# Kernel tuning notes

Hardware: AMD Instinct MI355X
Metric: run time of the kernel (lower is better)

Reference implementation:

```python
import jax, jax.numpy as jnp
import numpy as np
import math

# Module hyperparameters (from init_kwargs)
T_TOTAL = 1.0
NUM_STEPS = 8          # == len(F), number of time-indexed sub-networks (experts)
D = 1024               # feature dim (shape = [D])
DH = 4096              # hidden dim of each expert MLP
B = 4096               # batch size
H_STEP = T_TOTAL / NUM_STEPS
EIGMIN, EIGINIT, EIGMAX = -1.0, 0.0, 1.0   # spectral_limits=None
INV_SIG_099 = math.log(0.99 / (1 - 0.99))  # shifta/shiftb/scales init (learn flags False)


def setup_inputs() -> dict:
    key = jax.random.key(0)
    ks = jax.random.split(key, 8)
    t = jax.random.uniform(ks[0], (B,), dtype=jnp.float32) * T_TOTAL
    y = jax.random.normal(ks[1], (B, D), dtype=jnp.float32)
    # Per-expert 2-layer MLP params, stacked over the expert axis E
    s1 = 1.0 / math.sqrt(D)
    s2 = 1.0 / math.sqrt(DH)
    W1 = jax.random.normal(ks[2], (NUM_STEPS, D, DH), dtype=jnp.float32) * s1
    b1 = jnp.zeros((NUM_STEPS, DH), dtype=jnp.float32)
    W2 = jax.random.normal(ks[3], (NUM_STEPS, DH, D), dtype=jnp.float32) * s2
    b2 = jnp.zeros((NUM_STEPS, D), dtype=jnp.float32)
    scales = jnp.full((1, D), INV_SIG_099, dtype=jnp.float32)
    shifta = jnp.float32(INV_SIG_099)
    shiftb = jnp.float32(INV_SIG_099)
    return {"t": t, "y": y, "W1": W1, "b1": b1, "W2": W2, "b2": b2,
            "scales": scales, "shifta": shifta, "shiftb": shiftb}


def reference(t, y, W1, b1, W2, b2, scales, shifta, shiftb):
    E = W1.shape[0]
    # t2ind: per-sample expert index, clamped to the last expert
    ind = jnp.minimum((t / H_STEP).astype(jnp.int32), E - 1)          # [B]
    # Run every expert on every sample (dense dispatch), then gather per-sample result.
    hid = jnp.tanh(jnp.einsum('bd,edh->ebh', y, W1) + b1[:, None, :])  # [E,B,DH]
    fe = jnp.einsum('ebh,ehd->ebd', hid, W2) + b2[:, None, :]          # [E,B,D]
    f = jnp.take_along_axis(fe, ind[None, :, None].astype(jnp.int32), axis=0)[0]  # [B,D]
    f = jax.nn.sigmoid(scales) * f
    a = EIGINIT + jax.nn.sigmoid(shifta) * (EIGMIN - EIGINIT)
    b = EIGINIT + jax.nn.sigmoid(shiftb) * (EIGMAX - EIGINIT)
    return 0.5 * ((b - a) * f + (a + b) * y)
```

## Files before the change

kernel.cpp:

```cpp
#include <hip/hip_runtime.h>
#include <hip/hip_bf16.h>
#include <math.h>

#define NEXP 8
#define DIM_D 1024
#define DIM_H 4096
#define NB 4096

typedef __attribute__((ext_vector_type(8))) short short8;
typedef __attribute__((ext_vector_type(4))) float floatx4;

__device__ __forceinline__ unsigned short f2bf(float x) {
  __hip_bfloat16 h = __float2bfloat16(x);
  unsigned short u;
  __builtin_memcpy(&u, &h, 2);
  return u;
}
__device__ __forceinline__ unsigned int pack2bf(float a, float b) {
  return (unsigned int)f2bf(a) | ((unsigned int)f2bf(b) << 16);
}

__device__ __forceinline__ void async_copy16(const void* g, void* l) {
  __builtin_amdgcn_global_load_lds(
      (const __attribute__((address_space(1))) unsigned int*)g,
      (__attribute__((address_space(3))) unsigned int*)l, 16, 0, 0);
}

__global__ void setup_kernel(const float* __restrict__ t,
                             int* __restrict__ offs, int* __restrict__ perm) {
  __shared__ int cnt[NEXP];
  __shared__ int cur[NEXP];
  const int tid = threadIdx.x;
  if (tid < NEXP) cnt[tid] = 0;
  __syncthreads();
  for (int i = tid; i < NB; i += 256) {
    int e = (int)(t[i] * 8.0f);
    e = e < 0 ? 0 : (e > NEXP - 1 ? NEXP - 1 : e);
    atomicAdd(&cnt[e], 1);
  }
  __syncthreads();
  if (tid == 0) {
    int s = 0;
    for (int e = 0; e < NEXP; ++e) { offs[e] = s; cur[e] = s; s += cnt[e]; }
    offs[NEXP] = s;
  }
  __syncthreads();
  for (int i = tid; i < NB; i += 256) {
    int e = (int)(t[i] * 8.0f);
    e = e < 0 ? 0 : (e > NEXP - 1 ? NEXP - 1 : e);
    int slot = atomicAdd(&cur[e], 1);
    perm[slot] = i;
  }
}

__global__ __launch_bounds__(256)
void cvt_kernel(const float* __restrict__ in, __hip_bfloat16* __restrict__ out) {
  const long long i = ((long long)blockIdx.x * 256 + threadIdx.x) * 8;
  const float4 a = *(const float4*)(in + i);
  const float4 b = *(const float4*)(in + i + 4);
  unsigned int r[4];
  r[0] = pack2bf(a.x, a.y);
  r[1] = pack2bf(a.z, a.w);
  r[2] = pack2bf(b.x, b.y);
  r[3] = pack2bf(b.z, b.w);
  *(uint4*)(out + i) = *(const uint4*)r;
}

__global__ __launch_bounds__(256)
void transpose_cvt_kernel(const float* __restrict__ in,
                          __hip_bfloat16* __restrict__ out, int R, int C) {
  __shared__ unsigned int wbuf[32 * 69];
  const long long base = (long long)blockIdx.z * R * C;
  const int c0 = blockIdx.x * 64;
  const int r0 = blockIdx.y * 64;
  const int t = threadIdx.x;
  {
    const int p = t >> 3, g = t & 7;
    const float* s0 = in + base + (long long)(r0 + 2 * p) * C + c0 + g * 8;
    const float4 a0 = *(const float4*)(s0);
    const float4 a1 = *(const float4*)(s0 + 4);
    const float4 b0 = *(const float4*)(s0 + C);
    const float4 b1v = *(const float4*)(s0 + C + 4);
    unsigned int* dp = &wbuf[p * 69 + g * 8];
    dp[0] = pack2bf(a0.x, b0.x);
    dp[1] = pack2bf(a0.y, b0.y);
    dp[2] = pack2bf(a0.z, b0.z);
    dp[3] = pack2bf(a0.w, b0.w);
    dp[4] = pack2bf(a1.x, b1v.x);
    dp[5] = pack2bf(a1.y, b1v.y);
    dp[6] = pack2bf(a1.z, b1v.z);
    dp[7] = pack2bf(a1.w, b1v.w);
  }
  __syncthreads();
  {
    const int oc = t >> 2, rq = t & 3;
    __align__(16) unsigned int res[8];
#pragma unroll
    for (int j = 0; j < 8; ++j) res[j] = wbuf[(rq * 8 + j) * 69 + oc];
    __hip_bfloat16* dstp = out + base + (long long)(c0 + oc) * R + r0 + rq * 16;
    *(uint4*)dstp = *(const uint4*)&res[0];
    *(uint4*)(dstp + 8) = *(const uint4*)&res[4];
  }
}

template <int MODE>
__global__ __launch_bounds__(256, 2)
void gemm_kernel(const __hip_bfloat16* __restrict__ A,
                 const __hip_bfloat16* __restrict__ BT,
                 const float* __restrict__ bias,
                 const int* __restrict__ offs, const int* __restrict__ perm,
                 void* __restrict__ dstv,
                 const float* __restrict__ yin,
                 const float* __restrict__ scales,
                 const float* __restrict__ shifta,
                 const float* __restrict__ shiftb,
                 int K, int N) {
  const int e  = blockIdx.y >> 5;
  const int mt = blockIdx.y & 31;
  const int off = offs[e];
  const int cnt = offs[e + 1] - off;
  const int m0 = mt * 128;
  if (m0 >= cnt) return;
  const int rows = min(128, cnt - m0);
  const int n0 = blockIdx.x * 128;

  __shared__ __align__(16) char lds[65536];

  const int tid = threadIdx.x;
  const int w = tid >> 6, l = tid & 63;

  const __hip_bfloat16* aptr[4];
  const __hip_bfloat16* bptr[4];
#pragma unroll
  for (int j = 0; j < 4; ++j) {
    const int chunk = j * 256 + tid;
    const int cgrp = chunk >> 9;
    const int row  = (chunk >> 2) & 127;
    const int c2   = chunk & 3;
    const int ra = row < rows ? row : rows - 1;
    const long long ga = (MODE == 0) ? (long long)perm[off + m0 + ra]
                                     : (long long)(off + m0 + ra);
    aptr[j] = A + ga * K + cgrp * 32 + c2 * 8;
    bptr[j] = BT + ((long long)e * N + n0 + row) * K + cgrp * 32 + c2 * 8;
  }

  floatx4 acc[4][4];
#pragma unroll
  for (int i = 0; i < 4; ++i)
#pragma unroll
    for (int j = 0; j < 4; ++j) acc[i][j] = (floatx4){0.f, 0.f, 0.f, 0.f};

  const int wm = w >> 1, wn = w & 1;
  const int fr = l & 15;
  const int fq = l >> 4;
  const int ldsA = (wm * 64 + fr) * 64 + fq * 16;
  const int ldsB = 16384 + (wn * 64 + fr) * 64 + fq * 16;

  const int nt = K >> 6;

#pragma unroll
  for (int j = 0; j < 4; ++j) {
    async_copy16(aptr[j], lds + j * 4096 + w * 1024);
    async_copy16(bptr[j], lds + 16384 + j * 4096 + w * 1024);
    aptr[j] += 64; bptr[j] += 64;
  }
  __syncthreads();

  for (int t = 0; t < nt; ++t) {
    const int cur = (t & 1) << 15;
    if (t + 1 < nt) {
      const int nxt = cur ^ 32768;
#pragma unroll
      for (int j = 0; j < 4; ++j) {
        async_copy16(aptr[j], lds + nxt + j * 4096 + w * 1024);
        async_copy16(bptr[j], lds + nxt + 16384 + j * 4096 + w * 1024);
        aptr[j] += 64; bptr[j] += 64;
      }
    }
    short8 af[2][4], bf[2][4];
#pragma unroll
    for (int ks = 0; ks < 2; ++ks) {
#pragma unroll
      for (int mi = 0; mi < 4; ++mi)
        af[ks][mi] = *(const short8*)(lds + cur + ks * 8192 + mi * 1024 + ldsA);
#pragma unroll
      for (int ni = 0; ni < 4; ++ni)
        bf[ks][ni] = *(const short8*)(lds + cur + ks * 8192 + ni * 1024 + ldsB);
    }
#pragma unroll
    for (int ks = 0; ks < 2; ++ks)
#pragma unroll
      for (int mi = 0; mi < 4; ++mi)
#pragma unroll
        for (int ni = 0; ni < 4; ++ni)
          acc[mi][ni] = __builtin_amdgcn_mfma_f32_16x16x32_bf16(
              af[ks][mi], bf[ks][ni], acc[mi][ni], 0, 0, 0);
    if (t + 1 < nt) __syncthreads();
  }

  float av = 0.f, bv = 0.f;
  if (MODE == 1) {
    const float sa = 1.f / (1.f + expf(-shifta[0]));
    const float sb = 1.f / (1.f + expf(-shiftb[0]));
    av = 0.0f + sa * (-1.0f - 0.0f);
    bv = 0.0f + sb * (1.0f - 0.0f);
  }

#pragma unroll
  for (int mi = 0; mi < 4; ++mi) {
#pragma unroll
    for (int r = 0; r < 4; ++r) {
      const int rl = wm * 64 + mi * 16 + fq * 4 + r;
      if (rl >= rows) continue;
      const int i = off + m0 + rl;
      const int orig = (MODE == 1) ? perm[i] : 0;
#pragma unroll
      for (int ni = 0; ni < 4; ++ni) {
        const int cg = n0 + wn * 64 + ni * 16 + fr;
        const float x = acc[mi][ni][r] + bias[e * N + cg];
        if (MODE == 0) {
          ((__hip_bfloat16*)dstv)[(long long)i * N + cg] = __float2bfloat16(tanhf(x));
        } else {
          const float sc = 1.f / (1.f + expf(-scales[cg]));
          const float yv = yin[(long long)orig * N + cg];
          const float res = 0.5f * ((bv - av) * sc * x + (av + bv) * yv);
          ((float*)dstv)[(long long)orig * N + cg] = res;
        }
      }
    }
  }
}

extern "C" void kernel_launch(void* const* d_in, const int* in_sizes, int n_in,
                              void* d_out, int out_size, void* d_ws, size_t ws_size,
                              hipStream_t stream) {
  const float* t      = (const float*)d_in[0];
  const float* y      = (const float*)d_in[1];
  const float* W1     = (const float*)d_in[2];
  const float* b1     = (const float*)d_in[3];
  const float* W2     = (const float*)d_in[4];
  const float* b2     = (const float*)d_in[5];
  const float* scales = (const float*)d_in[6];
  const float* shifta = (const float*)d_in[7];
  const float* shiftb = (const float*)d_in[8];

  char* ws = (char*)d_ws;
  __hip_bfloat16* WT  = (__hip_bfloat16*)ws;
  __hip_bfloat16* hid = (__hip_bfloat16*)(ws + (size_t)64 * 1024 * 1024);
  __hip_bfloat16* ybf = (__hip_bfloat16*)(ws + (size_t)96 * 1024 * 1024);
  int* offs = (int*)(ws + (size_t)104 * 1024 * 1024);
  int* perm = offs + 16;

  setup_kernel<<<1, 256, 0, stream>>>(t, offs, perm);

  cvt_kernel<<<(NB * DIM_D) / (256 * 8), 256, 0, stream>>>(y, ybf);

  transpose_cvt_kernel<<<dim3(DIM_H / 64, DIM_D / 64, NEXP), 256, 0, stream>>>(
      W1, WT, DIM_D, DIM_H);
  gemm_kernel<0><<<dim3(DIM_H / 128, NEXP * 32), 256, 0, stream>>>(
      ybf, WT, b1, offs, perm, hid, nullptr, nullptr, nullptr, nullptr,
      DIM_D, DIM_H);
  transpose_cvt_kernel<<<dim3(DIM_D / 64, DIM_H / 64, NEXP), 256, 0, stream>>>(
      W2, WT, DIM_H, DIM_D);
  gemm_kernel<1><<<dim3(DIM_D / 128, NEXP * 32), 256, 0, stream>>>(
      hid, WT, b2, offs, perm, d_out, y, scales, shifta, shiftb,
      DIM_H, DIM_D);
}
```

Measured before the change: 494.1 us.

## Deepen GEMM pipeline to 4 LDS stages with XOR swizzle and XCD-aware block remap

Replaces the double-buffered K loop with a 4-buffer, 3-deep prefetch pipeline that uses explicit vmcnt waits and raw barriers. The LDS tile layout becomes a 128-byte-row layout with an XOR swizzle to avoid bank conflicts. Block indices are remapped so each XCD works on a contiguous slice of expert row tiles, which should improve L2 reuse. The gathered row indices are cached in LDS once per block. In exchange, LDS use doubles to 128KB and launch bounds drop to one block per CU, which lowers occupancy.

```diff
diff --git a/kernel.cpp b/kernel.cpp
--- a/kernel.cpp
+++ b/kernel.cpp
@@ -104,7 +104,7 @@
 }
 
 template <int MODE>
-__global__ __launch_bounds__(256, 2)
+__global__ __launch_bounds__(256, 1)
 void gemm_kernel(const __hip_bfloat16* __restrict__ A,
                  const __hip_bfloat16* __restrict__ BT,
                  const float* __restrict__ bias,
@@ -115,34 +115,55 @@
                  const float* __restrict__ shifta,
                  const float* __restrict__ shiftb,
                  int K, int N) {
-  const int e  = blockIdx.y >> 5;
-  const int mt = blockIdx.y & 31;
+  const int lin = blockIdx.x + gridDim.x * blockIdx.y;
+  const int xcd = lin & 7;
+  const int idx = lin >> 3;
+  const int gx = gridDim.x;
+  const int shift = (gx == 8) ? 3 : 5;
+  const int bx = idx & (gx - 1);
+  const int by = xcd * (gridDim.y >> 3) + (idx >> shift);
+
+  const int e  = by >> 5;
+  const int mt = by & 31;
   const int off = offs[e];
   const int cnt = offs[e + 1] - off;
   const int m0 = mt * 128;
   if (m0 >= cnt) return;
   const int rows = min(128, cnt - m0);
-  const int n0 = blockIdx.x * 128;
-
-  __shared__ __align__(16) char lds[65536];
+  const int n0 = bx * 128;
+
+  __shared__ __align__(16) char lds[131072];
+  __shared__ int rowmap[128];
 
   const int tid = threadIdx.x;
+  if (tid < 128) {
+    int r = tid < rows ? tid : rows - 1;
+    rowmap[tid] = (MODE == 0) ? perm[off + m0 + r] : (off + m0 + r);
+  }
+  __syncthreads();
+
   const int w = tid >> 6, l = tid & 63;
 
+  const int srow = tid >> 3;
+  const int kc = (tid & 7) ^ (srow & 7);
   const __hip_bfloat16* aptr[4];
   const __hip_bfloat16* bptr[4];
 #pragma unroll
   for (int j = 0; j < 4; ++j) {
-    const int chunk = j * 256 + tid;
-    const int cgrp = chunk >> 9;
-    const int row  = (chunk >> 2) & 127;
-    const int c2   = chunk & 3;
-    const int ra = row < rows ? row : rows - 1;
-    const long long ga = (MODE == 0) ? (long long)perm[off + m0 + ra]
-                                     : (long long)(off + m0 + ra);
-    aptr[j] = A + ga * K + cgrp * 32 + c2 * 8;
-    bptr[j] = BT + ((long long)e * N + n0 + row) * K + cgrp * 32 + c2 * 8;
-  }
+    const int row = j * 32 + srow;
+    aptr[j] = A + (long long)rowmap[row] * K + kc * 8;
+    bptr[j] = BT + ((long long)e * N + n0 + row) * K + kc * 8;
+  }
+
+  auto stage = [&](int buf) {
+    char* dst = lds + (buf << 15);
+#pragma unroll
+    for (int j = 0; j < 4; ++j) {
+      async_copy16(aptr[j], dst + j * 4096 + w * 1024);
+      async_copy16(bptr[j], dst + 16384 + j * 4096 + w * 1024);
+      aptr[j] += 64; bptr[j] += 64;
+    }
+  };
 
   floatx4 acc[4][4];
 #pragma unroll
@@ -153,50 +174,54 @@
   const int wm = w >> 1, wn = w & 1;
   const int fr = l & 15;
   const int fq = l >> 4;
-  const int ldsA = (wm * 64 + fr) * 64 + fq * 16;
-  const int ldsB = 16384 + (wn * 64 + fr) * 64 + fq * 16;
-
-  const int nt = K >> 6;
-
-#pragma unroll
-  for (int j = 0; j < 4; ++j) {
-    async_copy16(aptr[j], lds + j * 4096 + w * 1024);
-    async_copy16(bptr[j], lds + 16384 + j * 4096 + w * 1024);
-    aptr[j] += 64; bptr[j] += 64;
-  }
-  __syncthreads();
-
-  for (int t = 0; t < nt; ++t) {
-    const int cur = (t & 1) << 15;
-    if (t + 1 < nt) {
-      const int nxt = cur ^ 32768;
-#pragma unroll
-      for (int j = 0; j < 4; ++j) {
-        async_copy16(aptr[j], lds + nxt + j * 4096 + w * 1024);
-        async_copy16(bptr[j], lds + nxt + 16384 + j * 4096 + w * 1024);
-        aptr[j] += 64; bptr[j] += 64;
-      }
-    }
-    short8 af[2][4], bf[2][4];
+  const int fx = fr & 7;
+  int aoff[2], boff[2];
+#pragma unroll
+  for (int ks = 0; ks < 2; ++ks) {
+    aoff[ks] = (wm * 64 + fr) * 128 + (((ks * 4) | fq) ^ fx) * 16;
+    boff[ks] = 16384 + (wn * 64 + fr) * 128 + (((ks * 4) | fq) ^ fx) * 16;
+  }
+
+  auto compute = [&](int buf) {
+    const char* src = lds + (buf << 15);
 #pragma unroll
     for (int ks = 0; ks < 2; ++ks) {
+      short8 af[4], bf[4];
 #pragma unroll
       for (int mi = 0; mi < 4; ++mi)
-        af[ks][mi] = *(const short8*)(lds + cur + ks * 8192 + mi * 1024 + ldsA);
+        af[mi] = *(const short8*)(src + mi * 2048 + aoff[ks]);
 #pragma unroll
       for (int ni = 0; ni < 4; ++ni)
-        bf[ks][ni] = *(const short8*)(lds + cur + ks * 8192 + ni * 1024 + ldsB);
-    }
-#pragma unroll
-    for (int ks = 0; ks < 2; ++ks)
+        bf[ni] = *(const short8*)(src + ni * 2048 + boff[ks]);
 #pragma unroll
       for (int mi = 0; mi < 4; ++mi)
 #pragma unroll
         for (int ni = 0; ni < 4; ++ni)
           acc[mi][ni] = __builtin_amdgcn_mfma_f32_16x16x32_bf16(
-              af[ks][mi], bf[ks][ni], acc[mi][ni], 0, 0, 0);
-    if (t + 1 < nt) __syncthreads();
-  }
+              af[mi], bf[ni], acc[mi][ni], 0, 0, 0);
+    }
+  };
+
+  const int nt = K >> 6;
+
+  stage(0); stage(1); stage(2);
+
+#define K_ITER(T, WAITN)                                          \
+  do {                                                            \
+    asm volatile("s_waitcnt vmcnt(" #WAITN ")" ::: "memory");     \
+    __builtin_amdgcn_s_barrier();                                 \
+    __builtin_amdgcn_sched_barrier(0);                            \
+    if ((T) + 3 < nt) stage(((T) + 3) & 3);                       \
+    compute((T) & 3);                                             \
+    __builtin_amdgcn_sched_barrier(0);                            \
+    __builtin_amdgcn_s_barrier();                                 \
+  } while (0)
+
+  int t = 0;
+  for (; t < nt - 2; ++t) K_ITER(t, 16);
+  K_ITER(t, 8);  ++t;
+  K_ITER(t, 0);
+#undef K_ITER
 
   float av = 0.f, bv = 0.f;
   if (MODE == 1) {
```

Result: slower. 601.9 us (+21.8%).

## Add compact tile worklist and 4-stage swizzled LDS pipeline to grouped GEMM

Applied to the files above, without the earlier changes.

The setup kernel now builds a compact worklist of (expert, m-tile) pairs, so the grouped GEMMs launch 64 y-blocks instead of 256 mostly-empty ones. The GEMM main loop moves from a double-buffered K=64 step to a 4-deep ring of K=32 stages driven by explicit vmcnt waits and barriers. LDS rows are XOR-swizzled to avoid bank conflicts, and fragments are read with inline ds_read_b128. Gathered row indices are cached in shared memory. The worklist holds at most 64 tiles and silently drops any beyond that, and the hand-written waitcnt sequencing is fragile.

```diff
diff --git a/kernel.cpp b/kernel.cpp
--- a/kernel.cpp
+++ b/kernel.cpp
@@ -27,7 +27,8 @@
 }
 
 __global__ void setup_kernel(const float* __restrict__ t,
-                             int* __restrict__ offs, int* __restrict__ perm) {
+                             int* __restrict__ offs, int* __restrict__ perm,
+                             int* __restrict__ wl) {
   __shared__ int cnt[NEXP];
   __shared__ int cur[NEXP];
   const int tid = threadIdx.x;
@@ -43,6 +44,20 @@
     int s = 0;
     for (int e = 0; e < NEXP; ++e) { offs[e] = s; cur[e] = s; s += cnt[e]; }
     offs[NEXP] = s;
+    for (int i = 0; i < 64; ++i) wl[i] = -1;
+    for (int e = 0; e < NEXP; ++e) {
+      int tiles = (cnt[e] + 127) >> 7;
+      int lim = tiles < 8 ? tiles : 8;
+      for (int r = 0; r < lim; ++r) wl[r * 8 + e] = (r << 4) | e;
+    }
+    int free_s = 0;
+    for (int e = 0; e < NEXP; ++e) {
+      int tiles = (cnt[e] + 127) >> 7;
+      for (int r = 8; r < tiles; ++r) {
+        while (free_s < 64 && wl[free_s] >= 0) ++free_s;
+        if (free_s < 64) wl[free_s] = (r << 4) | e;
+      }
+    }
   }
   __syncthreads();
   for (int i = tid; i < NB; i += 256) {
@@ -109,14 +124,17 @@
                  const __hip_bfloat16* __restrict__ BT,
                  const float* __restrict__ bias,
                  const int* __restrict__ offs, const int* __restrict__ perm,
+                 const int* __restrict__ wl,
                  void* __restrict__ dstv,
                  const float* __restrict__ yin,
                  const float* __restrict__ scales,
                  const float* __restrict__ shifta,
                  const float* __restrict__ shiftb,
                  int K, int N) {
-  const int e  = blockIdx.y >> 5;
-  const int mt = blockIdx.y & 31;
+  const int wle = wl[blockIdx.y];
+  if (wle < 0) return;
+  const int e  = wle & 15;
+  const int mt = wle >> 4;
   const int off = offs[e];
   const int cnt = offs[e + 1] - off;
   const int m0 = mt * 128;
@@ -125,24 +143,38 @@
   const int n0 = blockIdx.x * 128;
 
   __shared__ __align__(16) char lds[65536];
+  __shared__ int rowmap[128];
 
   const int tid = threadIdx.x;
+  if (tid < 128) {
+    int r = tid < rows ? tid : rows - 1;
+    rowmap[tid] = (MODE == 0) ? perm[off + m0 + r] : (off + m0 + r);
+  }
+  __syncthreads();
+
   const int w = tid >> 6, l = tid & 63;
 
-  const __hip_bfloat16* aptr[4];
-  const __hip_bfloat16* bptr[4];
-#pragma unroll
-  for (int j = 0; j < 4; ++j) {
-    const int chunk = j * 256 + tid;
-    const int cgrp = chunk >> 9;
-    const int row  = (chunk >> 2) & 127;
-    const int c2   = chunk & 3;
-    const int ra = row < rows ? row : rows - 1;
-    const long long ga = (MODE == 0) ? (long long)perm[off + m0 + ra]
-                                     : (long long)(off + m0 + ra);
-    aptr[j] = A + ga * K + cgrp * 32 + c2 * 8;
-    bptr[j] = BT + ((long long)e * N + n0 + row) * K + cgrp * 32 + c2 * 8;
-  }
+  const int q_s = ((tid >> 2) & 3) ^ ((tid >> 4) & 3);
+  const int kc  = (tid & 3) ^ q_s;
+  const int r2  = tid >> 2;
+  const __hip_bfloat16* aptr[2];
+  const __hip_bfloat16* bptr[2];
+#pragma unroll
+  for (int i = 0; i < 2; ++i) {
+    const int row = i * 64 + r2;
+    aptr[i] = A + (long long)rowmap[row] * K + kc * 8;
+    bptr[i] = BT + ((long long)e * N + n0 + row) * K + kc * 8;
+  }
+
+  auto stage = [&](int buf) {
+    char* dst = lds + (buf << 14);
+#pragma unroll
+    for (int i = 0; i < 2; ++i) {
+      async_copy16(aptr[i], dst + i * 4096 + w * 1024);
+      async_copy16(bptr[i], dst + 8192 + i * 4096 + w * 1024);
+      aptr[i] += 32; bptr[i] += 32;
+    }
+  };
 
   floatx4 acc[4][4];
 #pragma unroll
@@ -153,50 +185,56 @@
   const int wm = w >> 1, wn = w & 1;
   const int fr = l & 15;
   const int fq = l >> 4;
-  const int ldsA = (wm * 64 + fr) * 64 + fq * 16;
-  const int ldsB = 16384 + (wn * 64 + fr) * 64 + fq * 16;
-
-  const int nt = K >> 6;
-
-#pragma unroll
-  for (int j = 0; j < 4; ++j) {
-    async_copy16(aptr[j], lds + j * 4096 + w * 1024);
-    async_copy16(bptr[j], lds + 16384 + j * 4096 + w * 1024);
-    aptr[j] += 64; bptr[j] += 64;
-  }
-  __syncthreads();
-
-  for (int t = 0; t < nt; ++t) {
-    const int cur = (t & 1) << 15;
-    if (t + 1 < nt) {
-      const int nxt = cur ^ 32768;
-#pragma unroll
-      for (int j = 0; j < 4; ++j) {
-        async_copy16(aptr[j], lds + nxt + j * 4096 + w * 1024);
-        async_copy16(bptr[j], lds + nxt + 16384 + j * 4096 + w * 1024);
-        aptr[j] += 64; bptr[j] += 64;
-      }
-    }
-    short8 af[2][4], bf[2][4];
-#pragma unroll
-    for (int ks = 0; ks < 2; ++ks) {
-#pragma unroll
-      for (int mi = 0; mi < 4; ++mi)
-        af[ks][mi] = *(const short8*)(lds + cur + ks * 8192 + mi * 1024 + ldsA);
+  const int slot = fq ^ ((fr & 3) ^ ((fr >> 2) & 3));
+  const unsigned lbase = (unsigned)(unsigned long long)
+      (__attribute__((address_space(3))) char*)lds;
+  const unsigned abase = lbase + (unsigned)((wm * 64 + fr) * 64 + slot * 16);
+  const unsigned bbase = lbase + 8192u + (unsigned)((wn * 64 + fr) * 64 + slot * 16);
+
+  auto compute = [&](int buf) {
+    const unsigned ab = abase + (unsigned)(buf << 14);
+    const unsigned bb = bbase + (unsigned)(buf << 14);
+    short8 af0, af1, af2, af3, bf0, bf1, bf2, bf3;
+    asm volatile("ds_read_b128 %0, %1" : "=v"(af0) : "v"(ab));
+    asm volatile("ds_read_b128 %0, %1 offset:1024" : "=v"(af1) : "v"(ab));
+    asm volatile("ds_read_b128 %0, %1 offset:2048" : "=v"(af2) : "v"(ab));
+    asm volatile("ds_read_b128 %0, %1 offset:3072" : "=v"(af3) : "v"(ab));
+    asm volatile("ds_read_b128 %0, %1" : "=v"(bf0) : "v"(bb));
+    asm volatile("ds_read_b128 %0, %1 offset:1024" : "=v"(bf1) : "v"(bb));
+    asm volatile("ds_read_b128 %0, %1 offset:2048" : "=v"(bf2) : "v"(bb));
+    asm volatile("ds_read_b128 %0, %1 offset:3072" : "=v"(bf3) : "v"(bb));
+    asm volatile("s_waitcnt lgkmcnt(0)" ::: "memory");
+    __builtin_amdgcn_sched_barrier(0);
+    short8 af[4] = {af0, af1, af2, af3};
+    short8 bf[4] = {bf0, bf1, bf2, bf3};
+#pragma unroll
+    for (int mi = 0; mi < 4; ++mi)
 #pragma unroll
       for (int ni = 0; ni < 4; ++ni)
-        bf[ks][ni] = *(const short8*)(lds + cur + ks * 8192 + ni * 1024 + ldsB);
-    }
-#pragma unroll
-    for (int ks = 0; ks < 2; ++ks)
-#pragma unroll
-      for (int mi = 0; mi < 4; ++mi)
-#pragma unroll
-        for (int ni = 0; ni < 4; ++ni)
-          acc[mi][ni] = __builtin_amdgcn_mfma_f32_16x16x32_bf16(
-              af[ks][mi], bf[ks][ni], acc[mi][ni], 0, 0, 0);
-    if (t + 1 < nt) __syncthreads();
-  }
+        acc[mi][ni] = __builtin_amdgcn_mfma_f32_16x16x32_bf16(
+            af[mi], bf[ni], acc[mi][ni], 0, 0, 0);
+  };
+
+  const int nt = K >> 5;
+
+  stage(0); stage(1); stage(2);
+
+  int t = 0;
+  for (; t < nt - 3; ++t) {
+    asm volatile("s_waitcnt vmcnt(8)" ::: "memory");
+    __builtin_amdgcn_s_barrier();
+    stage((t + 3) & 3);
+    compute(t & 3);
+  }
+  asm volatile("s_waitcnt vmcnt(8)" ::: "memory");
+  __builtin_amdgcn_s_barrier();
+  compute(t & 3); ++t;
+  asm volatile("s_waitcnt vmcnt(4)" ::: "memory");
+  __builtin_amdgcn_s_barrier();
+  compute(t & 3); ++t;
+  asm volatile("s_waitcnt vmcnt(0)" ::: "memory");
+  __builtin_amdgcn_s_barrier();
+  compute(t & 3);
 
   float av = 0.f, bv = 0.f;
   if (MODE == 1) {
@@ -250,19 +288,20 @@
   __hip_bfloat16* ybf = (__hip_bfloat16*)(ws + (size_t)96 * 1024 * 1024);
   int* offs = (int*)(ws + (size_t)104 * 1024 * 1024);
   int* perm = offs + 16;
-
-  setup_kernel<<<1, 256, 0, stream>>>(t, offs, perm);
+  int* wl   = perm + NB;
+
+  setup_kernel<<<1, 256, 0, stream>>>(t, offs, perm, wl);
 
   cvt_kernel<<<(NB * DIM_D) / (256 * 8), 256, 0, stream>>>(y, ybf);
 
   transpose_cvt_kernel<<<dim3(DIM_H / 64, DIM_D / 64, NEXP), 256, 0, stream>>>(
       W1, WT, DIM_D, DIM_H);
-  gemm_kernel<0><<<dim3(DIM_H / 128, NEXP * 32), 256, 0, stream>>>(
-      ybf, WT, b1, offs, perm, hid, nullptr, nullptr, nullptr, nullptr,
+  gemm_kernel<0><<<dim3(DIM_H / 128, 64), 256, 0, stream>>>(
+      ybf, WT, b1, offs, perm, wl, hid, nullptr, nullptr, nullptr, nullptr,
       DIM_D, DIM_H);
   transpose_cvt_kernel<<<dim3(DIM_D / 64, DIM_H / 64, NEXP), 256, 0, stream>>>(
       W2, WT, DIM_H, DIM_D);
-  gemm_kernel<1><<<dim3(DIM_D / 128, NEXP * 32), 256, 0, stream>>>(
-      hid, WT, b2, offs, perm, d_out, y, scales, shifta, shiftb,
+  gemm_kernel<1><<<dim3(DIM_D / 128, 64), 256, 0, stream>>>(
+      hid, WT, b2, offs, perm, wl, d_out, y, scales, shifta, shiftb,
       DIM_H, DIM_D);
 }
```

Result: slower. 505.3 us (+2.3%).
